# Kernel tuning notes

Hardware: AMD Instinct MI355X
Metric: run time of the kernel (lower is better)

Reference implementation:

```python
import math
import jax, jax.numpy as jnp
import numpy as np

B, S, H, D = 8, 2048, 16, 80
DM = H * D  # 1280 = input_dims


def setup_inputs() -> dict:
    key = jax.random.key(0)
    ks = jax.random.split(key, 10)
    s = 0.02
    return {
        "x": jax.random.normal(ks[0], (B, S, DM), dtype=jnp.float32),
        "Wq": jax.random.normal(ks[1], (DM, DM), dtype=jnp.float32) * s,
        "bq": jnp.zeros((DM,), dtype=jnp.float32),
        "Wk": jax.random.normal(ks[2], (DM, DM), dtype=jnp.float32) * s,
        "bk": jnp.zeros((DM,), dtype=jnp.float32),
        "Wv": jax.random.normal(ks[3], (DM, DM), dtype=jnp.float32) * s,
        "bv": jnp.zeros((DM,), dtype=jnp.float32),
        "Wp": jax.random.normal(ks[4], (DM, DM), dtype=jnp.float32) * s,
        "bp": jnp.zeros((DM,), dtype=jnp.float32),
        "per_dim_scale": jnp.ones((D,), dtype=jnp.float32),
    }


def reference(x, Wq, bq, Wk, bk, Wv, bv, Wp, bp, per_dim_scale):
    # Projections: [B,S,DM] -> [B,S,H,D]
    q = (x @ Wq + bq).reshape(B, S, H, D)
    k = (x @ Wk + bk).reshape(B, S, H, D)
    v = (x @ Wv + bv).reshape(B, S, H, D)
    # Faithful to source: matmul over last two dims of (B,S,H,D) tensors,
    # i.e. scores are [B,S,H,H] -- mixing across HEADS at each position.
    scale = 1.0 / math.sqrt(D)
    attn = jnp.einsum('bshd,bstd->bsht', q, k) * scale  # [B,S,H,H]
    attn = jax.nn.softmax(attn, axis=-1)
    out = jnp.einsum('bsht,bstd->bshd', attn, v)  # [B,S,H,D]
    out = out * per_dim_scale  # broadcast over D
    out = out.reshape(B, S, DM)
    return out @ Wp + bp
```

## Files before the change

### kernel.cpp

```cpp
#include <hip/hip_runtime.h>
#include <hip/hip_bf16.h>

#define M_TOT   16384
#define DMODEL  1280
#define NHEAD   16
#define DHEAD   80
#define NTC     5
#define BK      64
#define NKT     (DMODEL / BK)

typedef __attribute__((ext_vector_type(8))) __bf16 bf16x8;
typedef __attribute__((ext_vector_type(4))) float  f32x4;

__device__ __forceinline__ void gload16(const void* g, void* l) {
  __builtin_amdgcn_global_load_lds(
      (const __attribute__((address_space(1))) void*)g,
      (__attribute__((address_space(3))) void*)l, 16, 0, 0);
}

__device__ __forceinline__ float bf2f(unsigned short u) {
  return __uint_as_float((unsigned)u << 16);
}

__global__ __launch_bounds__(256) void cvt_bf16_kernel(
    const float* __restrict__ x, __hip_bfloat16* __restrict__ y, int n4) {
  int i = blockIdx.x * 256 + threadIdx.x;
  if (i >= n4) return;
  float4 v = ((const float4*)x)[i];
  union { ushort4 u; __hip_bfloat16 h[4]; } o;
  o.h[0] = __float2bfloat16(v.x);
  o.h[1] = __float2bfloat16(v.y);
  o.h[2] = __float2bfloat16(v.z);
  o.h[3] = __float2bfloat16(v.w);
  ((ushort4*)y)[i] = o.u;
}

__global__ __launch_bounds__(256) void transpose_cvt_kernel(
    const float* __restrict__ W0, const float* __restrict__ W1,
    const float* __restrict__ W2, const float* __restrict__ W3,
    const float* __restrict__ pds,
    __hip_bfloat16* __restrict__ T0, __hip_bfloat16* __restrict__ T1,
    __hip_bfloat16* __restrict__ T2, __hip_bfloat16* __restrict__ T3) {
  const float* W = blockIdx.z == 0 ? W0 : blockIdx.z == 1 ? W1
                 : blockIdx.z == 2 ? W2 : W3;
  __hip_bfloat16* T = blockIdx.z == 0 ? T0 : blockIdx.z == 1 ? T1
                    : blockIdx.z == 2 ? T2 : T3;
  __shared__ float tile[32][33];
  int bx = blockIdx.x * 32, by = blockIdx.y * 32;
  int tx = threadIdx.x, ty = threadIdx.y;
  for (int j = 0; j < 32; j += 8)
    tile[ty + j][tx] = W[(size_t)(by + ty + j) * DMODEL + bx + tx];
  __syncthreads();
  const float scale = (blockIdx.z == 3) ? pds[(by + tx) % DHEAD] : 1.0f;
  for (int j = 0; j < 32; j += 8)
    T[(size_t)(bx + ty + j) * DMODEL + by + tx] =
        __float2bfloat16(tile[tx][ty + j] * scale);
}

#define MFMA16(AF, BF, MB)                                                   \
  do {                                                                       \
    _Pragma("unroll")                                                        \
    for (int j_ = 0; j_ < 4; ++j_) {                                         \
      _Pragma("unroll")                                                      \
      for (int n_ = 0; n_ < 4; ++n_)                                         \
        acc[(MB) + j_][n_] = __builtin_amdgcn_mfma_f32_16x16x32_bf16(        \
            AF[j_], BF[n_], acc[(MB) + j_][n_], 0, 0, 0);                    \
    }                                                                        \
  } while (0)

template <bool OUT_BF16>
__global__ __launch_bounds__(512, 2) void gemm_bt_kernel(
    const __hip_bfloat16* __restrict__ A,
    const __hip_bfloat16* __restrict__ Bt0,
    const __hip_bfloat16* __restrict__ Bt1,
    const __hip_bfloat16* __restrict__ Bt2,
    const float* __restrict__ bias0, const float* __restrict__ bias1,
    const float* __restrict__ bias2,
    void* __restrict__ C0, void* __restrict__ C1, void* __restrict__ C2) {
  const int mat   = blockIdx.y / NTC;
  const int ntile = blockIdx.y % NTC;
  const __hip_bfloat16* Bt = mat == 0 ? Bt0 : mat == 1 ? Bt1 : Bt2;
  const float* bias        = mat == 0 ? bias0 : mat == 1 ? bias1 : bias2;
  void* C                  = mat == 0 ? C0 : mat == 1 ? C1 : C2;

  const int bm = blockIdx.x * 256;
  const int bn = ntile * 256;

  __shared__ __align__(16) char SLDS[131072];

  const int tid  = threadIdx.x;
  const int lane = tid & 63;
  const int wid  = tid >> 6;
  const int wm   = (wid >> 2) * 128;
  const int wn   = (wid & 3) * 64;
  const int lrow = lane & 15;
  const int l4   = lane >> 4;

  const int rsub  = lane >> 2;
  const int cswz  = (lane & 3) ^ ((rsub >> 1) & 3);
  const char* gsrc[2][2][2];
#pragma unroll
  for (int i = 0; i < 2; ++i) {
    const int rA = bm + wid * 32 + i * 16 + rsub;
    const int rB = bn + wid * 32 + i * 16 + rsub;
#pragma unroll
    for (int s = 0; s < 2; ++s) {
      gsrc[0][i][s] = (const char*)A  + (size_t)rA * (DMODEL * 2) + s * 64 + cswz * 16;
      gsrc[1][i][s] = (const char*)Bt + (size_t)rB * (DMODEL * 2) + s * 64 + cswz * 16;
    }
  }

  auto issueGroup = [&](int M, int s, int nbuf, size_t koff) {
    char* d = SLDS + M * 65536 + nbuf * 32768 + s * 16384 + wid * 2048;
    gload16(gsrc[M][0][s] + koff, d);
    gload16(gsrc[M][1][s] + koff, d + 1024);
  };

  f32x4 acc[8][4];
#pragma unroll
  for (int i = 0; i < 8; ++i)
#pragma unroll
    for (int j = 0; j < 4; ++j) acc[i][j] = (f32x4){0.f, 0.f, 0.f, 0.f};

  const int swz  = ((l4 ^ ((lrow >> 1) & 3)) << 4);
  const int aOff = (wm + lrow) * 64 + swz;
  const int bOff = 65536 + (wn + lrow) * 64 + swz;

  issueGroup(0, 0, 0, 0);
  issueGroup(1, 0, 0, 0);
  issueGroup(0, 1, 0, 0);
  issueGroup(1, 1, 0, 0);
  asm volatile("s_waitcnt vmcnt(4)" ::: "memory");
  __builtin_amdgcn_s_barrier();

  bf16x8 aFa[4], aFb[4], aFc[4], aFd[4], bF0[4], bF1[4];
#pragma unroll
  for (int j = 0; j < 4; ++j) aFa[j] = *(const bf16x8*)(const void*)(SLDS + aOff + j * 1024);
#pragma unroll
  for (int n = 0; n < 4; ++n) bF0[n] = *(const bf16x8*)(const void*)(SLDS + bOff + n * 1024);
  __builtin_amdgcn_sched_barrier(0);

  for (int t = 0; t < NKT; ++t) {
    const int buf = t & 1, nbuf = buf ^ 1;
    const int b0 = buf << 15;
    const int n0 = nbuf << 15;
    const size_t koff = (size_t)(t + 1) * (BK * 2);
    const bool pf = (t + 1 < NKT);

    __builtin_amdgcn_s_barrier();
#pragma unroll
    for (int j = 0; j < 4; ++j)
      aFb[j] = *(const bf16x8*)(const void*)(SLDS + b0 + aOff + (4 + j) * 1024);
    if (pf) issueGroup(0, 0, nbuf, koff);
    __builtin_amdgcn_sched_barrier(0);
    __builtin_amdgcn_s_setprio(1);
    MFMA16(aFa, bF0, 0);
    __builtin_amdgcn_s_setprio(0);
    __builtin_amdgcn_sched_barrier(0);

    if (pf) asm volatile("s_waitcnt vmcnt(2)" ::: "memory");
    else    asm volatile("s_waitcnt vmcnt(0)" ::: "memory");
    __builtin_amdgcn_s_barrier();
#pragma unroll
    for (int j = 0; j < 4; ++j)
      aFc[j] = *(const bf16x8*)(const void*)(SLDS + b0 + 16384 + aOff + j * 1024);
#pragma unroll
    for (int n = 0; n < 4; ++n)
      bF1[n] = *(const bf16x8*)(const void*)(SLDS + b0 + 16384 + bOff + n * 1024);
    if (pf) issueGroup(1, 0, nbuf, koff);
    __builtin_amdgcn_sched_barrier(0);
    __builtin_amdgcn_s_setprio(1);
    MFMA16(aFb, bF0, 4);
    __builtin_amdgcn_s_setprio(0);
    __builtin_amdgcn_sched_barrier(0);

    __builtin_amdgcn_s_barrier();
#pragma unroll
    for (int j = 0; j < 4; ++j)
      aFd[j] = *(const bf16x8*)(const void*)(SLDS + b0 + 16384 + aOff + (4 + j) * 1024);
    if (pf) issueGroup(0, 1, nbuf, koff);
    __builtin_amdgcn_sched_barrier(0);
    __builtin_amdgcn_s_setprio(1);
    MFMA16(aFc, bF1, 0);
    __builtin_amdgcn_s_setprio(0);
    __builtin_amdgcn_sched_barrier(0);

    if (pf) asm volatile("s_waitcnt vmcnt(2)" ::: "memory");
    __builtin_amdgcn_s_barrier();
    if (pf) {
#pragma unroll
      for (int j = 0; j < 4; ++j)
        aFa[j] = *(const bf16x8*)(const void*)(SLDS + n0 + aOff + j * 1024);
#pragma unroll
      for (int n = 0; n < 4; ++n)
        bF0[n] = *(const bf16x8*)(const void*)(SLDS + n0 + bOff + n * 1024);
      issueGroup(1, 1, nbuf, koff);
    }
    __builtin_amdgcn_sched_barrier(0);
    __builtin_amdgcn_s_setprio(1);
    MFMA16(aFd, bF1, 4);
    __builtin_amdgcn_s_setprio(0);
    __builtin_amdgcn_sched_barrier(0);
  }

  const int rbase = l4 * 4;
#pragma unroll
  for (int mi = 0; mi < 8; ++mi) {
#pragma unroll
    for (int ni = 0; ni < 4; ++ni) {
      const int col = bn + wn + ni * 16 + lrow;
      const float b2 = bias[col];
#pragma unroll
      for (int r = 0; r < 4; ++r) {
        const int row = bm + wm + mi * 16 + rbase + r;
        const float val = acc[mi][ni][r] + b2;
        if (OUT_BF16)
          ((__hip_bfloat16*)C)[(size_t)row * DMODEL + col] = __float2bfloat16(val);
        else
          ((float*)C)[(size_t)row * DMODEL + col] = val;
      }
    }
  }
}

__global__ __launch_bounds__(256, 2) void gemm_bt128_kernel(
    const __hip_bfloat16* __restrict__ A,
    const __hip_bfloat16* __restrict__ Bt,
    const float* __restrict__ bias,
    float* __restrict__ C) {
  const int bm = blockIdx.x * 128;
  const int bn = blockIdx.y * 128;

  __shared__ __align__(16) char SLDS[65536];

  const int tid  = threadIdx.x;
  const int lane = tid & 63;
  const int wid  = tid >> 6;
  const int wm   = (wid >> 1) * 64;
  const int wn   = (wid & 1) * 64;
  const int lrow = lane & 15;
  const int l4   = lane >> 4;

  const int rsub  = lane >> 2;
  const int cswz  = (lane & 3) ^ ((rsub >> 1) & 3);
  const char* gsrc[2][2][2];
#pragma unroll
  for (int i = 0; i < 2; ++i) {
    const int rA = bm + wid * 32 + i * 16 + rsub;
    const int rB = bn + wid * 32 + i * 16 + rsub;
#pragma unroll
    for (int s = 0; s < 2; ++s) {
      gsrc[0][i][s] = (const char*)A  + (size_t)rA * (DMODEL * 2) + s * 64 + cswz * 16;
      gsrc[1][i][s] = (const char*)Bt + (size_t)rB * (DMODEL * 2) + s * 64 + cswz * 16;
    }
  }

  auto issueGroup = [&](int M, int s, int nbuf, size_t koff) {
    char* d = SLDS + M * 32768 + nbuf * 16384 + s * 8192 + wid * 2048;
    gload16(gsrc[M][0][s] + koff, d);
    gload16(gsrc[M][1][s] + koff, d + 1024);
  };

  f32x4 acc[4][4];
#pragma unroll
  for (int i = 0; i < 4; ++i)
#pragma unroll
    for (int j = 0; j < 4; ++j) acc[i][j] = (f32x4){0.f, 0.f, 0.f, 0.f};

  const int swz  = ((l4 ^ ((lrow >> 1) & 3)) << 4);
  const int aOff = (wm + lrow) * 64 + swz;
  const int bOff = 32768 + (wn + lrow) * 64 + swz;

  issueGroup(0, 0, 0, 0);
  issueGroup(1, 0, 0, 0);
  issueGroup(0, 1, 0, 0);
  issueGroup(1, 1, 0, 0);

  for (int t = 0; t < NKT; ++t) {
    const int buf = t & 1, nbuf = buf ^ 1;
    const int b0 = buf << 14;
    const size_t koff = (size_t)(t + 1) * (BK * 2);
    const bool pf = (t + 1 < NKT);

    asm volatile("s_waitcnt vmcnt(4)" ::: "memory");
    __builtin_amdgcn_s_barrier();
    bf16x8 aF[4], bF[4];
#pragma unroll
    for (int j = 0; j < 4; ++j)
      aF[j] = *(const bf16x8*)(const void*)(SLDS + b0 + aOff + j * 1024);
#pragma unroll
    for (int n = 0; n < 4; ++n)
      bF[n] = *(const bf16x8*)(const void*)(SLDS + b0 + bOff + n * 1024);
    if (pf) { issueGroup(0, 0, nbuf, koff); issueGroup(1, 0, nbuf, koff); }
    __builtin_amdgcn_sched_barrier(0);
    __builtin_amdgcn_s_setprio(1);
    MFMA16(aF, bF, 0);
    __builtin_amdgcn_s_setprio(0);
    __builtin_amdgcn_sched_barrier(0);

    if (pf) asm volatile("s_waitcnt vmcnt(4)" ::: "memory");
    else    asm volatile("s_waitcnt vmcnt(0)" ::: "memory");
    __builtin_amdgcn_s_barrier();
#pragma unroll
    for (int j = 0; j < 4; ++j)
      aF[j] = *(const bf16x8*)(const void*)(SLDS + b0 + 8192 + aOff + j * 1024);
#pragma unroll
    for (int n = 0; n < 4; ++n)
      bF[n] = *(const bf16x8*)(const void*)(SLDS + b0 + 8192 + bOff + n * 1024);
    if (pf) { issueGroup(0, 1, nbuf, koff); issueGroup(1, 1, nbuf, koff); }
    __builtin_amdgcn_sched_barrier(0);
    __builtin_amdgcn_s_setprio(1);
    MFMA16(aF, bF, 0);
    __builtin_amdgcn_s_setprio(0);
    __builtin_amdgcn_sched_barrier(0);
  }

  const int rbase = l4 * 4;
#pragma unroll
  for (int mi = 0; mi < 4; ++mi) {
#pragma unroll
    for (int ni = 0; ni < 4; ++ni) {
      const int col = bn + wn + ni * 16 + lrow;
      const float bb = bias[col];
#pragma unroll
      for (int r = 0; r < 4; ++r) {
        const int row = bm + wm + mi * 16 + rbase + r;
        C[(size_t)row * DMODEL + col] = acc[mi][ni][r] + bb;
      }
    }
  }
}

__global__ __launch_bounds__(256) void attn_kernel(
    const __hip_bfloat16* __restrict__ q, const __hip_bfloat16* __restrict__ k,
    const __hip_bfloat16* __restrict__ v,
    __hip_bfloat16* __restrict__ out) {
  const size_t base = (size_t)blockIdx.x * DMODEL;
  __shared__ float qs[16][84], ks[16][84], vs[16][84];
  __shared__ float ps[16][17];
  const int tid = threadIdx.x;

  for (int c = tid; c < 480; c += 256) {
    int matid = c / 160, idx = c - matid * 160;
    int h = idx / 10, d0 = (idx - h * 10) * 8;
    const __hip_bfloat16* src = matid == 0 ? q : matid == 1 ? k : v;
    union { bf16x8 v8; unsigned short u[8]; } uu;
    uu.v8 = *(const bf16x8*)(const void*)(src + base + (size_t)idx * 8);
    float* dst = (matid == 0 ? &qs[0][0] : matid == 1 ? &ks[0][0] : &vs[0][0]) +
                 h * 84 + d0;
#pragma unroll
    for (int j = 0; j < 8; ++j) dst[j] = bf2f(uu.u[j]);
  }
  __syncthreads();

  const int h = tid >> 4, t = tid & 15;
  float s = 0.f;
#pragma unroll
  for (int d = 0; d < DHEAD; ++d) s += qs[h][d] * ks[t][d];
  s *= 0.11180339887498948f;

  float m = s;
#pragma unroll
  for (int off = 8; off; off >>= 1) m = fmaxf(m, __shfl_xor(m, off, 16));
  float e = expf(s - m);
  float sum = e;
#pragma unroll
  for (int off = 8; off; off >>= 1) sum += __shfl_xor(sum, off, 16);
  ps[h][t] = e / sum;
  __syncthreads();

  {
    const int hh   = tid >> 4;
    const int dloc = (tid & 15) * 5;
    float o[5];
#pragma unroll
    for (int j = 0; j < 5; ++j) o[j] = 0.f;
#pragma unroll
    for (int tt = 0; tt < 16; ++tt) {
      const float p = ps[hh][tt];
#pragma unroll
      for (int j = 0; j < 5; ++j) o[j] += p * vs[tt][dloc + j];
    }
    __hip_bfloat16* ob = out + base + (size_t)hh * DHEAD + dloc;
#pragma unroll
    for (int j = 0; j < 5; ++j) ob[j] = __float2bfloat16(o[j]);
  }
}

extern "C" void kernel_launch(void* const* d_in, const int* in_sizes, int n_in,
                              void* d_out, int out_size, void* d_ws, size_t ws_size,
                              hipStream_t stream) {
  const float* x   = (const float*)d_in[0];
  const float* Wq  = (const float*)d_in[1];
  const float* bq  = (const float*)d_in[2];
  const float* Wk  = (const float*)d_in[3];
  const float* bk  = (const float*)d_in[4];
  const float* Wv  = (const float*)d_in[5];
  const float* bv  = (const float*)d_in[6];
  const float* Wp  = (const float*)d_in[7];
  const float* bp  = (const float*)d_in[8];
  const float* pds = (const float*)d_in[9];
  float* out = (float*)d_out;

  char* ws = (char*)d_ws;
  const size_t ACT = (size_t)M_TOT * DMODEL * 2;
  const size_t WT  = (size_t)DMODEL * DMODEL * 2;
  __hip_bfloat16* xbf = (__hip_bfloat16*)(ws);
  __hip_bfloat16* qbf = (__hip_bfloat16*)(ws + ACT);
  __hip_bfloat16* kbf = (__hip_bfloat16*)(ws + 2 * ACT);
  __hip_bfloat16* vbf = (__hip_bfloat16*)(ws + 3 * ACT);
  __hip_bfloat16* wtq = (__hip_bfloat16*)(ws + 4 * ACT);
  __hip_bfloat16* wtk = (__hip_bfloat16*)(ws + 4 * ACT + WT);
  __hip_bfloat16* wtv = (__hip_bfloat16*)(ws + 4 * ACT + 2 * WT);
  __hip_bfloat16* wtp = (__hip_bfloat16*)(ws + 4 * ACT + 3 * WT);
  __hip_bfloat16* attnbf = xbf;

  {
    int n4 = (M_TOT * DMODEL) / 4;
    cvt_bf16_kernel<<<n4 / 256, 256, 0, stream>>>(x, xbf, n4);
  }
  {
    dim3 g(DMODEL / 32, DMODEL / 32, 4), b(32, 8);
    transpose_cvt_kernel<<<g, b, 0, stream>>>(Wq, Wk, Wv, Wp, pds,
                                              wtq, wtk, wtv, wtp);
  }
  {
    dim3 g(M_TOT / 256, 3 * NTC);
    gemm_bt_kernel<true><<<g, 512, 0, stream>>>(
        xbf, wtq, wtk, wtv, bq, bk, bv, (void*)qbf, (void*)kbf, (void*)vbf);
  }
  attn_kernel<<<M_TOT, 256, 0, stream>>>(qbf, kbf, vbf, attnbf);
  {
    dim3 g(M_TOT / 128, DMODEL / 128);
    gemm_bt128_kernel<<<g, 256, 0, stream>>>(attnbf, wtp, bp, out);
  }
}
```

Before: 306.2 us.

## Restructure GEMM main loop into two phases with fewer barriers

Reorganizes the K-loop of the bf16 GEMM from four barrier-separated quarter-phases into two half-phases. Each half loads a full k-half of fragments (A upper/lower and B) and runs two MFMA blocks back to back. It also drops the sched_barrier fences so the compiler can interleave LDS reads with MFMAs. This is meant to cut barrier and sync overhead, at the cost of higher register pressure from more live fragments and less explicit control over scheduling.

```diff
diff --git a/kernel.cpp b/kernel.cpp
--- a/kernel.cpp
+++ b/kernel.cpp
@@ -135,10 +135,14 @@
 
   bf16x8 aFa[4], aFb[4], aFc[4], aFd[4], bF0[4], bF1[4];
 #pragma unroll
-  for (int j = 0; j < 4; ++j) aFa[j] = *(const bf16x8*)(const void*)(SLDS + aOff + j * 1024);
-#pragma unroll
-  for (int n = 0; n < 4; ++n) bF0[n] = *(const bf16x8*)(const void*)(SLDS + bOff + n * 1024);
-  __builtin_amdgcn_sched_barrier(0);
+  for (int j = 0; j < 4; ++j)
+    aFa[j] = *(const bf16x8*)(const void*)(SLDS + aOff + j * 1024);
+#pragma unroll
+  for (int n = 0; n < 4; ++n)
+    bF0[n] = *(const bf16x8*)(const void*)(SLDS + bOff + n * 1024);
+#pragma unroll
+  for (int j = 0; j < 4; ++j)
+    aFb[j] = *(const bf16x8*)(const void*)(SLDS + aOff + (4 + j) * 1024);
 
   for (int t = 0; t < NKT; ++t) {
     const int buf = t & 1, nbuf = buf ^ 1;
@@ -147,60 +151,47 @@
     const size_t koff = (size_t)(t + 1) * (BK * 2);
     const bool pf = (t + 1 < NKT);
 
+    if (pf) {
+      issueGroup(0, 0, nbuf, koff);
+      asm volatile("s_waitcnt vmcnt(2)" ::: "memory");
+    } else {
+      asm volatile("s_waitcnt vmcnt(0)" ::: "memory");
+    }
     __builtin_amdgcn_s_barrier();
 #pragma unroll
     for (int j = 0; j < 4; ++j)
-      aFb[j] = *(const bf16x8*)(const void*)(SLDS + b0 + aOff + (4 + j) * 1024);
-    if (pf) issueGroup(0, 0, nbuf, koff);
-    __builtin_amdgcn_sched_barrier(0);
+      aFc[j] = *(const bf16x8*)(const void*)(SLDS + b0 + 16384 + aOff + j * 1024);
+#pragma unroll
+    for (int n = 0; n < 4; ++n)
+      bF1[n] = *(const bf16x8*)(const void*)(SLDS + b0 + 16384 + bOff + n * 1024);
+#pragma unroll
+    for (int j = 0; j < 4; ++j)
+      aFd[j] = *(const bf16x8*)(const void*)(SLDS + b0 + 16384 + aOff + (4 + j) * 1024);
+    if (pf) issueGroup(1, 0, nbuf, koff);
     __builtin_amdgcn_s_setprio(1);
     MFMA16(aFa, bF0, 0);
-    __builtin_amdgcn_s_setprio(0);
-    __builtin_amdgcn_sched_barrier(0);
-
-    if (pf) asm volatile("s_waitcnt vmcnt(2)" ::: "memory");
-    else    asm volatile("s_waitcnt vmcnt(0)" ::: "memory");
-    __builtin_amdgcn_s_barrier();
-#pragma unroll
-    for (int j = 0; j < 4; ++j)
-      aFc[j] = *(const bf16x8*)(const void*)(SLDS + b0 + 16384 + aOff + j * 1024);
-#pragma unroll
-    for (int n = 0; n < 4; ++n)
-      bF1[n] = *(const bf16x8*)(const void*)(SLDS + b0 + 16384 + bOff + n * 1024);
-    if (pf) issueGroup(1, 0, nbuf, koff);
-    __builtin_amdgcn_sched_barrier(0);
-    __builtin_amdgcn_s_setprio(1);
     MFMA16(aFb, bF0, 4);
     __builtin_amdgcn_s_setprio(0);
-    __builtin_amdgcn_sched_barrier(0);
-
-    __builtin_amdgcn_s_barrier();
-#pragma unroll
-    for (int j = 0; j < 4; ++j)
-      aFd[j] = *(const bf16x8*)(const void*)(SLDS + b0 + 16384 + aOff + (4 + j) * 1024);
-    if (pf) issueGroup(0, 1, nbuf, koff);
-    __builtin_amdgcn_sched_barrier(0);
+
+    if (pf) {
+      issueGroup(0, 1, nbuf, koff);
+      asm volatile("s_waitcnt vmcnt(2)" ::: "memory");
+      __builtin_amdgcn_s_barrier();
+#pragma unroll
+      for (int j = 0; j < 4; ++j)
+        aFa[j] = *(const bf16x8*)(const void*)(SLDS + n0 + aOff + j * 1024);
+#pragma unroll
+      for (int n = 0; n < 4; ++n)
+        bF0[n] = *(const bf16x8*)(const void*)(SLDS + n0 + bOff + n * 1024);
+#pragma unroll
+      for (int j = 0; j < 4; ++j)
+        aFb[j] = *(const bf16x8*)(const void*)(SLDS + n0 + aOff + (4 + j) * 1024);
+      issueGroup(1, 1, nbuf, koff);
+    }
     __builtin_amdgcn_s_setprio(1);
     MFMA16(aFc, bF1, 0);
-    __builtin_amdgcn_s_setprio(0);
-    __builtin_amdgcn_sched_barrier(0);
-
-    if (pf) asm volatile("s_waitcnt vmcnt(2)" ::: "memory");
-    __builtin_amdgcn_s_barrier();
-    if (pf) {
-#pragma unroll
-      for (int j = 0; j < 4; ++j)
-        aFa[j] = *(const bf16x8*)(const void*)(SLDS + n0 + aOff + j * 1024);
-#pragma unroll
-      for (int n = 0; n < 4; ++n)
-        bF0[n] = *(const bf16x8*)(const void*)(SLDS + n0 + bOff + n * 1024);
-      issueGroup(1, 1, nbuf, koff);
-    }
-    __builtin_amdgcn_sched_barrier(0);
-    __builtin_amdgcn_s_setprio(1);
     MFMA16(aFd, bF1, 4);
     __builtin_amdgcn_s_setprio(0);
-    __builtin_amdgcn_sched_barrier(0);
   }
 
   const int rbase = l4 * 4;
```

Result: no change. 307.4 us (+0.4%).
